# Performance work log

Hardware: AMD Instinct MI355X
Metric: run time of the kernel (lower is better)

## Reference

```python
import jax, jax.numpy as jnp
import numpy as np

B, T, D = 2048, 60, 6
H, F, O = 64, 10, 1


def setup_inputs() -> dict:
    key = jax.random.key(0)
    ks = jax.random.split(key, 16)
    w = lambda k, shape, s=0.1: jax.random.normal(k, shape, jnp.float32) * s
    return {
        "x": jax.random.normal(ks[0], (B, T, D), jnp.float32),
        "W_i": w(ks[1], (D, H)), "U_i": w(ks[2], (H, H)), "b_i": jnp.zeros((H,), jnp.float32),
        "W_ste": w(ks[3], (D, H)), "U_ste": w(ks[4], (H, H)), "b_ste": jnp.ones((H,), jnp.float32),
        "W_fre": w(ks[5], (D, F)), "U_fre": w(ks[6], (H, F)), "b_fre": jnp.ones((F,), jnp.float32),
        "W_c": w(ks[7], (D, H)), "U_c": w(ks[8], (H, H)), "b_c": jnp.zeros((H,), jnp.float32),
        "W_o": w(ks[9], (D, H)), "U_o": w(ks[10], (H, H)), "b_o": jnp.zeros((H,), jnp.float32),
        "U_a": w(ks[11], (F, 1)), "b_a": jnp.zeros((H,), jnp.float32),
        "W_p": w(ks[12], (H, O)), "b_p": jnp.zeros((O,), jnp.float32),
    }


def _hsig(v):
    # torch.nn.Hardsigmoid: relu6(x + 3) / 6
    return jnp.clip(v / 6.0 + 0.5, 0.0, 1.0)


def reference(x, W_i, U_i, b_i, W_ste, U_ste, b_ste, W_fre, U_fre, b_fre,
              W_c, U_c, b_c, W_o, U_o, b_o, U_a, b_a, W_p, b_p):
    b, t_len, _ = x.shape
    h_dim = W_i.shape[1]
    f_dim = W_fre.shape[1]
    freq = jnp.arange(f_dim, dtype=x.dtype) / f_dim  # (F,)
    ua = U_a[:, 0]  # (F,)

    def step(carry, x_t):
        h, S_re, S_im, t = carry
        i = _hsig(x_t @ W_i + b_i + h @ U_i)              # (B,H)
        ste = _hsig(x_t @ W_ste + b_ste + h @ U_ste)      # (B,H)
        fre = _hsig(x_t @ W_fre + b_fre + h @ U_fre)      # (B,F)
        f = ste[:, :, None] * fre[:, None, :]             # (B,H,F)
        c = i * jnp.tanh(x_t @ W_c + b_c + h @ U_c)       # (B,H)
        t = t + 1.0
        omega = (2.0 * jnp.pi) * t * freq                  # (F,)
        S_re = f * S_re + c[:, :, None] * jnp.cos(omega)   # (B,H,F)
        S_im = f * S_im + c[:, :, None] * jnp.sin(omega)   # (B,H,F)
        A = S_re * S_re + S_im * S_im                      # (B,H,F)
        a = jnp.tanh(jnp.einsum('bhf,f->bh', A, ua) + b_a)
        o = _hsig(x_t @ W_o + b_o + h @ U_o)
        h = o * a
        return (h, S_re, S_im, t), None

    init = (jnp.zeros((b, h_dim), x.dtype),
            jnp.zeros((b, h_dim, f_dim), x.dtype),
            jnp.zeros((b, h_dim, f_dim), x.dtype),
            jnp.asarray(0.0, x.dtype))
    (h, _, _, _), _ = jax.lax.scan(step, init, jnp.swapaxes(x, 0, 1))
    # original returns p from the last timestep only
    return h @ W_p + b_p
```

## Files before the change

kernel.cpp:

```cpp
#include <hip/hip_runtime.h>


#define BB 2048
#define TT 60
#define DD 6
#define HH 64
#define FF 10
#define NB 8

#define XS 968
#define HS 72

typedef short bf16x8 __attribute__((ext_vector_type(8)));
typedef float f32x4  __attribute__((ext_vector_type(4)));

__device__ __forceinline__ unsigned short f2bf(float f) {
    union { float f; unsigned u; } v; v.f = f;
    unsigned r = v.u + 0x7fffu + ((v.u >> 16) & 1u);
    return (unsigned short)(r >> 16);
}
__device__ __forceinline__ float bf2f(unsigned short b) {
    union { unsigned u; float f; } v; v.u = ((unsigned)b) << 16; return v.f;
}
__device__ __forceinline__ float hsig_f(float v) {
    return __builtin_amdgcn_fmed3f(fmaf(v, 0.16666666666666666f, 0.5f), 0.0f, 1.0f);
}
__device__ __forceinline__ float tanh_f(float x) {
    float xc = fminf(fmaxf(x, -12.0f), 12.0f);
    float e  = __builtin_amdgcn_exp2f(xc * 2.8853900817779268f);
    return (e - 1.0f) * __builtin_amdgcn_rcpf(e + 1.0f);
}
__device__ __forceinline__ float uni(float v) {
    return __int_as_float(__builtin_amdgcn_readfirstlane(__float_as_int(v)));
}
__device__ __forceinline__ void pinv(bf16x8& v) { asm volatile("" : "+v"(v)); }

__global__ __launch_bounds__(512, 2)
void sfm_kernel(
    const float* __restrict__ x,
    const float* __restrict__ W_i,  const float* __restrict__ U_i,  const float* __restrict__ b_i,
    const float* __restrict__ W_ste,const float* __restrict__ U_ste,const float* __restrict__ b_ste,
    const float* __restrict__ W_fre,const float* __restrict__ U_fre,const float* __restrict__ b_fre,
    const float* __restrict__ W_c,  const float* __restrict__ U_c,  const float* __restrict__ b_c,
    const float* __restrict__ W_o,  const float* __restrict__ U_o,  const float* __restrict__ b_o,
    const float* __restrict__ U_a,  const float* __restrict__ b_a,
    const float* __restrict__ W_p,  const float* __restrict__ b_p,
    float* __restrict__ out)
{
    const int tid  = threadIdx.x;
    const int lane = tid & 63;
    const int wave = tid >> 6;
    const int q    = lane >> 4;
    const int n16  = lane & 15;
    const int b0   = blockIdx.x * NB;

    __shared__ __align__(16) unsigned short xsp[NB * XS];
    __shared__ __align__(16) unsigned short hhi[NB * HS];
    __shared__ __align__(16) unsigned short hlo[NB * HS];
    __shared__ __align__(16) float zbuf[4 * 64 * NB];
    __shared__ __align__(16) float frebuf[16 * NB];
    __shared__ float red[8][NB];

    if (tid < NB * TT) {
        const float* xg = x + (size_t)b0 * (TT * DD) + tid * DD;
        const int b = tid / TT, s = tid - b * TT;
        unsigned short* dst = &xsp[b * XS + s * 16];
        #pragma unroll
        for (int d = 0; d < DD; ++d) {
            const float v = xg[d];
            const unsigned short hb = f2bf(v);
            dst[d]     = hb;
            dst[8 + d] = f2bf(v - bf2f(hb));
        }
        dst[6] = 0x3F80; dst[7] = 0;
        dst[14] = 0; dst[15] = 0;
    }
    for (int i = tid; i < NB * HS; i += 512) { hhi[i] = 0; hlo[i] = 0; }

    const int g = wave >> 1;
    const int colbase = (wave & 1) * 32;
    const float* Ug = (g == 0) ? U_i : (g == 1) ? U_ste : (g == 2) ? U_c : U_o;
    const float* Wg = (g == 0) ? W_i : (g == 1) ? W_ste : (g == 2) ? W_c : W_o;
    const float* bg = (g == 0) ? b_i : (g == 1) ? b_ste : (g == 2) ? b_c : b_o;

    bf16x8 Bh[3][3], Bl[3][3];
    #pragma unroll
    for (int t = 0; t < 3; ++t) {
        #pragma unroll
        for (int c = 0; c < 3; ++c) {
            #pragma unroll
            for (int j = 0; j < 8; ++j) {
                const int kv = c * 32 + q * 8 + j;
                float v = 0.0f;
                if (t < 2) {
                    const int n = colbase + t * 16 + n16;
                    if      (kv < 64)  v = Ug[kv * HH + n];
                    else if (kv < 70)  v = Wg[(kv - 64) * HH + n];
                    else if (kv == 70) v = bg[n];
                } else if (wave == 7 && n16 < FF) {
                    if      (kv < 64)  v = U_fre[kv * FF + n16];
                    else if (kv < 70)  v = W_fre[(kv - 64) * FF + n16];
                    else if (kv == 70) v = b_fre[n16];
                }
                const unsigned short hb = f2bf(v);
                Bh[t][c][j] = (short)hb;
                Bl[t][c][j] = (short)f2bf(v - bf2f(hb));
            }
            pinv(Bh[t][c]); pinv(Bl[t][c]);
        }
    }

    const int pb = tid & (NB - 1);
    const int pc = tid >> 3;
    const float bav = b_a[pc];
    const float wpv = W_p[pc];
    const float bpv = uni(b_p[0]);
    float uav[FF];
    #pragma unroll
    for (int f = 0; f < FF; ++f) uav[f] = uni(U_a[f]);

    const float CBt[FF] = { 1.0f,  0.8090169943749475f,  0.30901699437494745f,
                           -0.30901699437494745f, -0.8090169943749475f, -1.0f,
                           -0.8090169943749475f, -0.30901699437494745f,
                            0.30901699437494745f,  0.8090169943749475f };
    const float SBt[FF] = { 0.0f,  0.5877852522924731f,  0.9510565162951535f,
                            0.9510565162951535f,  0.5877852522924731f,  0.0f,
                           -0.5877852522924731f, -0.9510565162951535f,
                           -0.9510565162951535f, -0.5877852522924731f };

    float Sre[FF], Sim[FF], cs[FF], sn[FF];
    #pragma unroll
    for (int f = 0; f < FF; ++f) {
        Sre[f] = 0.0f; Sim[f] = 0.0f; cs[f] = CBt[f]; sn[f] = SBt[f];
    }
    float hv = 0.0f;

    const int ab = n16 & (NB - 1);
    const unsigned short* hhp = &hhi[ab * HS];
    const unsigned short* hlp = &hlo[ab * HS];
    const unsigned short* xrow = &xsp[ab * XS];

    __syncthreads();

    int sm = 0;
    for (int s = 0; s < TT; ++s) {
        bf16x8 Ah[3], Al[3];
        #pragma unroll
        for (int c = 0; c < 2; ++c) {
            Ah[c] = *(const bf16x8*)&hhp[c * 32 + q * 8];
            Al[c] = *(const bf16x8*)&hlp[c * 32 + q * 8];
        }
        {
            const bf16x8 xvh = *(const bf16x8*)&xrow[s * 16];
            const bf16x8 xvl = *(const bf16x8*)&xrow[s * 16 + 8];
            const bf16x8 zf = {0, 0, 0, 0, 0, 0, 0, 0};
            Ah[2] = (q == 0) ? xvh : zf;
            Al[2] = (q == 0) ? xvl : zf;
        }

        f32x4 acc0 = {0.f,0.f,0.f,0.f}, acc1 = acc0, acc2 = acc0;
        #pragma unroll
        for (int c = 0; c < 3; ++c) {
            #pragma unroll
            for (int tm = 0; tm < 3; ++tm) {
                const bf16x8 a = (tm == 0) ? Al[c] : Ah[c];
                acc0 = __builtin_amdgcn_mfma_f32_16x16x32_bf16(a, (tm==1) ? Bl[0][c] : Bh[0][c], acc0, 0, 0, 0);
                acc1 = __builtin_amdgcn_mfma_f32_16x16x32_bf16(a, (tm==1) ? Bl[1][c] : Bh[1][c], acc1, 0, 0, 0);
                if (wave == 7)
                    acc2 = __builtin_amdgcn_mfma_f32_16x16x32_bf16(a, (tm==1) ? Bl[2][c] : Bh[2][c], acc2, 0, 0, 0);
            }
        }

        if (q < 2) {
            const int base = (g * 64 + colbase + n16) * NB + q * 4;
            *(f32x4*)&zbuf[base]          = acc0;
            *(f32x4*)&zbuf[base + 16*NB]  = acc1;
            if (wave == 7)
                *(f32x4*)&frebuf[n16 * NB + q * 4] = acc2;
        }
        __syncthreads();

        const float zi = zbuf[(0 * 64 + pc) * NB + pb];
        const float zs = zbuf[(1 * 64 + pc) * NB + pb];
        const float zc = zbuf[(2 * 64 + pc) * NB + pb];
        const float zo = zbuf[(3 * 64 + pc) * NB + pb];
        float fr[FF];
        #pragma unroll
        for (int f = 0; f < FF; ++f) fr[f] = hsig_f(frebuf[f * NB + pb]);

        const float iv  = hsig_f(zi);
        const float stv = hsig_f(zs);
        const float ov  = hsig_f(zo);
        const float cv  = iv * tanh_f(zc);

        if (sm == 0) {
            #pragma unroll
            for (int f = 0; f < FF; ++f) { cs[f] = CBt[f]; sn[f] = SBt[f]; }
        }

        float aacc = bav;
        #pragma unroll
        for (int f = 0; f < FF; ++f) {
            const float fc = stv * fr[f];
            Sre[f] = fmaf(fc, Sre[f], cv * cs[f]);
            Sim[f] = fmaf(fc, Sim[f], cv * sn[f]);
            const float A = fmaf(Sim[f], Sim[f], Sre[f] * Sre[f]);
            aacc = fmaf(A, uav[f], aacc);
            const float cc = cs[f];
            cs[f] = fmaf(cc, CBt[f], -(sn[f] * SBt[f]));
            sn[f] = fmaf(cc, SBt[f],   sn[f] * CBt[f]);
        }
        hv = ov * tanh_f(aacc);

        {
            const unsigned short hb = f2bf(hv);
            hhi[pb * HS + pc] = hb;
            hlo[pb * HS + pc] = f2bf(hv - bf2f(hb));
        }
        if (++sm == 10) sm = 0;
        __syncthreads();
    }

    float val = hv * wpv;
    val += __shfl_xor(val, 8, 64);
    val += __shfl_xor(val, 16, 64);
    val += __shfl_xor(val, 32, 64);
    if (lane < NB) red[wave][lane] = val;
    __syncthreads();
    if (tid < NB) {
        float acc = bpv;
        #pragma unroll
        for (int w = 0; w < 8; ++w) acc += red[w][tid];
        out[b0 + tid] = acc;
    }
}

extern "C" void kernel_launch(void* const* d_in, const int* in_sizes, int n_in,
                              void* d_out, int out_size, void* d_ws, size_t ws_size,
                              hipStream_t stream) {
    (void)in_sizes; (void)n_in; (void)d_ws; (void)ws_size; (void)out_size;
    const float* x     = (const float*)d_in[0];
    const float* W_i   = (const float*)d_in[1];
    const float* U_i   = (const float*)d_in[2];
    const float* b_i   = (const float*)d_in[3];
    const float* W_ste = (const float*)d_in[4];
    const float* U_ste = (const float*)d_in[5];
    const float* b_ste = (const float*)d_in[6];
    const float* W_fre = (const float*)d_in[7];
    const float* U_fre = (const float*)d_in[8];
    const float* b_fre = (const float*)d_in[9];
    const float* W_c   = (const float*)d_in[10];
    const float* U_c   = (const float*)d_in[11];
    const float* b_c   = (const float*)d_in[12];
    const float* W_o   = (const float*)d_in[13];
    const float* U_o   = (const float*)d_in[14];
    const float* b_o   = (const float*)d_in[15];
    const float* U_a   = (const float*)d_in[16];
    const float* b_a   = (const float*)d_in[17];
    const float* W_p   = (const float*)d_in[18];
    const float* b_p   = (const float*)d_in[19];

    sfm_kernel<<<BB / NB, 512, 0, stream>>>(
        x, W_i, U_i, b_i, W_ste, U_ste, b_ste, W_fre, U_fre, b_fre,
        W_c, U_c, b_c, W_o, U_o, b_o, U_a, b_a, W_p, b_p, (float*)d_out);
}
```

Baseline: 163.7 us.

## Transpose MFMA roles: weights as A operand, hi/lo hidden state stacked in N

Swaps the MFMA operands so the weight tiles are held in registers as the A operand. The hidden state's bf16 hi and lo halves are stacked as 16 N-columns, and the two partial sums are added when the gate inputs are read back. This drops from 9 MFMAs per tile to 6 per step and removes the per-lane A-fragment gathers. It also replaces the per-step cos/sin rotation recurrence with a shared-memory lookup table, splits the attention accumulation into two chains, and lowers the launch-bounds occupancy hint from 2 to 1. In exchange it adds an extra shared-memory read per gate, a shuffle for the frequency gate, and table loads in the inner loop.

```diff
diff --git a/kernel.cpp b/kernel.cpp
--- a/kernel.cpp
+++ b/kernel.cpp
@@ -9,7 +9,8 @@
 #define NB 8
 
 #define XS 968
-#define HS 72
+#define HSK 72
+#define ZC 68
 
 typedef short bf16x8 __attribute__((ext_vector_type(8)));
 typedef float f32x4  __attribute__((ext_vector_type(4)));
@@ -35,7 +36,7 @@
 }
 __device__ __forceinline__ void pinv(bf16x8& v) { asm volatile("" : "+v"(v)); }
 
-__global__ __launch_bounds__(512, 2)
+__global__ __launch_bounds__(512, 1)
 void sfm_kernel(
     const float* __restrict__ x,
     const float* __restrict__ W_i,  const float* __restrict__ U_i,  const float* __restrict__ b_i,
@@ -55,11 +56,12 @@
     const int b0   = blockIdx.x * NB;
 
     __shared__ __align__(16) unsigned short xsp[NB * XS];
-    __shared__ __align__(16) unsigned short hhi[NB * HS];
-    __shared__ __align__(16) unsigned short hlo[NB * HS];
-    __shared__ __align__(16) float zbuf[4 * 64 * NB];
-    __shared__ __align__(16) float frebuf[16 * NB];
-    __shared__ float red[8][NB];
+    __shared__ __align__(16) unsigned short hsp2[16 * HSK];
+    __shared__ __align__(16) float zt[4 * 16 * ZC];
+    __shared__ __align__(16) float fb[NB * 12];
+    __shared__ __align__(16) float ctab[10 * 10 * 2];
+    __shared__ float cstabB[10 * 2];
+    __shared__ float red[8][8];
 
     if (tid < NB * TT) {
         const float* xg = x + (size_t)b0 * (TT * DD) + tid * DD;
@@ -75,42 +77,65 @@
         dst[6] = 0x3F80; dst[7] = 0;
         dst[14] = 0; dst[15] = 0;
     }
-    for (int i = tid; i < NB * HS; i += 512) { hhi[i] = 0; hlo[i] = 0; }
-
-    const int g = wave >> 1;
-    const int colbase = (wave & 1) * 32;
-    const float* Ug = (g == 0) ? U_i : (g == 1) ? U_ste : (g == 2) ? U_c : U_o;
-    const float* Wg = (g == 0) ? W_i : (g == 1) ? W_ste : (g == 2) ? W_c : W_o;
-    const float* bg = (g == 0) ? b_i : (g == 1) ? b_ste : (g == 2) ? b_c : b_o;
-
-    bf16x8 Bh[3][3], Bl[3][3];
+    if (tid < 10) {
+        const float CTc[10] = { 1.0f,  0.8090169943749475f,  0.30901699437494745f,
+                               -0.30901699437494745f, -0.8090169943749475f, -1.0f,
+                               -0.8090169943749475f, -0.30901699437494745f,
+                                0.30901699437494745f,  0.8090169943749475f };
+        const float STc[10] = { 0.0f,  0.5877852522924731f,  0.9510565162951535f,
+                                0.9510565162951535f,  0.5877852522924731f,  0.0f,
+                               -0.5877852522924731f, -0.9510565162951535f,
+                               -0.9510565162951535f, -0.5877852522924731f };
+        float cc = 0.0f, ss = 0.0f;
+        #pragma unroll
+        for (int j = 0; j < 10; ++j) if (tid == j) { cc = CTc[j]; ss = STc[j]; }
+        cstabB[tid * 2] = cc; cstabB[tid * 2 + 1] = ss;
+    }
+    for (int i = tid; i < 16 * HSK; i += 512) hsp2[i] = 0;
+    __syncthreads();
+    if (tid < 100) {
+        const int mm = tid / 10, ff = tid - mm * 10;
+        const int idx = (ff * mm) % 10;
+        ctab[tid * 2]     = cstabB[idx * 2];
+        ctab[tid * 2 + 1] = cstabB[idx * 2 + 1];
+    }
+
+    const int NTILE = (wave == 7) ? 3 : 2;
+    bf16x8 Ah[3][3], Al[3][3];
     #pragma unroll
     for (int t = 0; t < 3; ++t) {
+        if (t >= NTILE) continue;
+        const bool isfre = (wave == 7 && t == 2);
+        const int gt = 2 * wave + t;
+        const int g  = gt >> 2, mt = gt & 3;
+        const int col = mt * 16 + n16;
+        const float* Ug = (g == 0) ? U_i : (g == 1) ? U_ste : (g == 2) ? U_c : U_o;
+        const float* Wg = (g == 0) ? W_i : (g == 1) ? W_ste : (g == 2) ? W_c : W_o;
+        const float* bg = (g == 0) ? b_i : (g == 1) ? b_ste : (g == 2) ? b_c : b_o;
         #pragma unroll
         for (int c = 0; c < 3; ++c) {
             #pragma unroll
             for (int j = 0; j < 8; ++j) {
                 const int kv = c * 32 + q * 8 + j;
                 float v = 0.0f;
-                if (t < 2) {
-                    const int n = colbase + t * 16 + n16;
-                    if      (kv < 64)  v = Ug[kv * HH + n];
-                    else if (kv < 70)  v = Wg[(kv - 64) * HH + n];
-                    else if (kv == 70) v = bg[n];
-                } else if (wave == 7 && n16 < FF) {
+                if (!isfre) {
+                    if      (kv < 64)  v = Ug[kv * HH + col];
+                    else if (kv < 70)  v = Wg[(kv - 64) * HH + col];
+                    else if (kv == 70) v = bg[col];
+                } else if (n16 < FF) {
                     if      (kv < 64)  v = U_fre[kv * FF + n16];
                     else if (kv < 70)  v = W_fre[(kv - 64) * FF + n16];
                     else if (kv == 70) v = b_fre[n16];
                 }
                 const unsigned short hb = f2bf(v);
-                Bh[t][c][j] = (short)hb;
-                Bl[t][c][j] = (short)f2bf(v - bf2f(hb));
+                Ah[t][c][j] = (short)hb;
+                Al[t][c][j] = (short)f2bf(v - bf2f(hb));
             }
-            pinv(Bh[t][c]); pinv(Bl[t][c]);
-        }
-    }
-
-    const int pb = tid & (NB - 1);
+            pinv(Ah[t][c]); pinv(Al[t][c]);
+        }
+    }
+
+    const int pb = tid & 7;
     const int pc = tid >> 3;
     const float bav = b_a[pc];
     const float wpv = W_p[pc];
@@ -119,105 +144,93 @@
     #pragma unroll
     for (int f = 0; f < FF; ++f) uav[f] = uni(U_a[f]);
 
-    const float CBt[FF] = { 1.0f,  0.8090169943749475f,  0.30901699437494745f,
-                           -0.30901699437494745f, -0.8090169943749475f, -1.0f,
-                           -0.8090169943749475f, -0.30901699437494745f,
-                            0.30901699437494745f,  0.8090169943749475f };
-    const float SBt[FF] = { 0.0f,  0.5877852522924731f,  0.9510565162951535f,
-                            0.9510565162951535f,  0.5877852522924731f,  0.0f,
-                           -0.5877852522924731f, -0.9510565162951535f,
-                           -0.9510565162951535f, -0.5877852522924731f };
-
-    float Sre[FF], Sim[FF], cs[FF], sn[FF];
+    float Sre[FF], Sim[FF];
     #pragma unroll
-    for (int f = 0; f < FF; ++f) {
-        Sre[f] = 0.0f; Sim[f] = 0.0f; cs[f] = CBt[f]; sn[f] = SBt[f];
-    }
+    for (int f = 0; f < FF; ++f) { Sre[f] = 0.0f; Sim[f] = 0.0f; }
     float hv = 0.0f;
 
-    const int ab = n16 & (NB - 1);
-    const unsigned short* hhp = &hhi[ab * HS];
-    const unsigned short* hlp = &hlo[ab * HS];
-    const unsigned short* xrow = &xsp[ab * XS];
+    const unsigned short* hrp = &hsp2[n16 * HSK];
+    const unsigned short* xrp = &xsp[(n16 & 7) * XS + (n16 >> 3) * 8];
 
     __syncthreads();
 
-    int sm = 0;
+    int m = 1;
     for (int s = 0; s < TT; ++s) {
-        bf16x8 Ah[3], Al[3];
-        #pragma unroll
-        for (int c = 0; c < 2; ++c) {
-            Ah[c] = *(const bf16x8*)&hhp[c * 32 + q * 8];
-            Al[c] = *(const bf16x8*)&hlp[c * 32 + q * 8];
-        }
-        {
-            const bf16x8 xvh = *(const bf16x8*)&xrow[s * 16];
-            const bf16x8 xvl = *(const bf16x8*)&xrow[s * 16 + 8];
-            const bf16x8 zf = {0, 0, 0, 0, 0, 0, 0, 0};
-            Ah[2] = (q == 0) ? xvh : zf;
-            Al[2] = (q == 0) ? xvl : zf;
-        }
-
-        f32x4 acc0 = {0.f,0.f,0.f,0.f}, acc1 = acc0, acc2 = acc0;
-        #pragma unroll
-        for (int c = 0; c < 3; ++c) {
+        const bf16x8 B0 = *(const bf16x8*)&hrp[q * 8];
+        const bf16x8 B1 = *(const bf16x8*)&hrp[32 + q * 8];
+        const bf16x8 xv = *(const bf16x8*)&xrp[s * 16];
+        const bf16x8 zf = {0, 0, 0, 0, 0, 0, 0, 0};
+        const bf16x8 B2 = (q == 0) ? xv : zf;
+
+        f32x4 acc[3];
+        #pragma unroll
+        for (int t = 0; t < 3; ++t) {
+            if (t >= NTILE) continue;
+            f32x4 a = {0.0f, 0.0f, 0.0f, 0.0f};
+            a = __builtin_amdgcn_mfma_f32_16x16x32_bf16(Ah[t][0], B0, a, 0, 0, 0);
+            a = __builtin_amdgcn_mfma_f32_16x16x32_bf16(Al[t][0], B0, a, 0, 0, 0);
+            a = __builtin_amdgcn_mfma_f32_16x16x32_bf16(Ah[t][1], B1, a, 0, 0, 0);
+            a = __builtin_amdgcn_mfma_f32_16x16x32_bf16(Al[t][1], B1, a, 0, 0, 0);
+            a = __builtin_amdgcn_mfma_f32_16x16x32_bf16(Ah[t][2], B2, a, 0, 0, 0);
+            a = __builtin_amdgcn_mfma_f32_16x16x32_bf16(Al[t][2], B2, a, 0, 0, 0);
+            acc[t] = a;
+        }
+
+        #pragma unroll
+        for (int t = 0; t < 2; ++t) {
+            const int gt = 2 * wave + t;
+            const int g  = gt >> 2, mt = gt & 3;
+            *(f32x4*)&zt[(g * 16 + n16) * ZC + mt * 16 + q * 4] = acc[t];
+        }
+        if (wave == 7) {
+            f32x4 af;
             #pragma unroll
-            for (int tm = 0; tm < 3; ++tm) {
-                const bf16x8 a = (tm == 0) ? Al[c] : Ah[c];
-                acc0 = __builtin_amdgcn_mfma_f32_16x16x32_bf16(a, (tm==1) ? Bl[0][c] : Bh[0][c], acc0, 0, 0, 0);
-                acc1 = __builtin_amdgcn_mfma_f32_16x16x32_bf16(a, (tm==1) ? Bl[1][c] : Bh[1][c], acc1, 0, 0, 0);
-                if (wave == 7)
-                    acc2 = __builtin_amdgcn_mfma_f32_16x16x32_bf16(a, (tm==1) ? Bl[2][c] : Bh[2][c], acc2, 0, 0, 0);
+            for (int r = 0; r < 4; ++r)
+                af[r] = acc[2][r] + __shfl_xor(acc[2][r], 8, 64);
+            if (n16 < 8) {
+                #pragma unroll
+                for (int r = 0; r < 4; ++r) {
+                    const int f = q * 4 + r;
+                    if (f < FF) fb[n16 * 12 + f] = af[r];
+                }
             }
         }
-
-        if (q < 2) {
-            const int base = (g * 64 + colbase + n16) * NB + q * 4;
-            *(f32x4*)&zbuf[base]          = acc0;
-            *(f32x4*)&zbuf[base + 16*NB]  = acc1;
-            if (wave == 7)
-                *(f32x4*)&frebuf[n16 * NB + q * 4] = acc2;
-        }
         __syncthreads();
 
-        const float zi = zbuf[(0 * 64 + pc) * NB + pb];
-        const float zs = zbuf[(1 * 64 + pc) * NB + pb];
-        const float zc = zbuf[(2 * 64 + pc) * NB + pb];
-        const float zo = zbuf[(3 * 64 + pc) * NB + pb];
+        const float zi = zt[(0 * 16 + pb) * ZC + pc] + zt[(0 * 16 + pb + 8) * ZC + pc];
+        const float zs = zt[(1 * 16 + pb) * ZC + pc] + zt[(1 * 16 + pb + 8) * ZC + pc];
+        const float zc = zt[(2 * 16 + pb) * ZC + pc] + zt[(2 * 16 + pb + 8) * ZC + pc];
+        const float zo = zt[(3 * 16 + pb) * ZC + pc] + zt[(3 * 16 + pb + 8) * ZC + pc];
+
         float fr[FF];
         #pragma unroll
-        for (int f = 0; f < FF; ++f) fr[f] = hsig_f(frebuf[f * NB + pb]);
+        for (int f = 0; f < FF; ++f) fr[f] = hsig_f(fb[pb * 12 + f]);
 
         const float iv  = hsig_f(zi);
         const float stv = hsig_f(zs);
         const float ov  = hsig_f(zo);
         const float cv  = iv * tanh_f(zc);
 
-        if (sm == 0) {
-            #pragma unroll
-            for (int f = 0; f < FF; ++f) { cs[f] = CBt[f]; sn[f] = SBt[f]; }
-        }
-
-        float aacc = bav;
+        const float* tp = &ctab[m * 20];
+        float aacc0 = bav, aacc1 = 0.0f;
         #pragma unroll
         for (int f = 0; f < FF; ++f) {
+            const float2 tv = *(const float2*)&tp[f * 2];
             const float fc = stv * fr[f];
-            Sre[f] = fmaf(fc, Sre[f], cv * cs[f]);
-            Sim[f] = fmaf(fc, Sim[f], cv * sn[f]);
+            Sre[f] = fmaf(fc, Sre[f], cv * tv.x);
+            Sim[f] = fmaf(fc, Sim[f], cv * tv.y);
             const float A = fmaf(Sim[f], Sim[f], Sre[f] * Sre[f]);
-            aacc = fmaf(A, uav[f], aacc);
-            const float cc = cs[f];
-            cs[f] = fmaf(cc, CBt[f], -(sn[f] * SBt[f]));
-            sn[f] = fmaf(cc, SBt[f],   sn[f] * CBt[f]);
-        }
-        hv = ov * tanh_f(aacc);
+            if (f & 1) aacc1 = fmaf(A, uav[f], aacc1);
+            else       aacc0 = fmaf(A, uav[f], aacc0);
+        }
+        hv = ov * tanh_f(aacc0 + aacc1);
 
         {
             const unsigned short hb = f2bf(hv);
-            hhi[pb * HS + pc] = hb;
-            hlo[pb * HS + pc] = f2bf(hv - bf2f(hb));
-        }
-        if (++sm == 10) sm = 0;
+            hsp2[pb * HSK + pc]       = hb;
+            hsp2[(8 + pb) * HSK + pc] = f2bf(hv - bf2f(hb));
+        }
+        if (++m == 10) m = 0;
         __syncthreads();
     }
 
@@ -225,7 +238,7 @@
     val += __shfl_xor(val, 8, 64);
     val += __shfl_xor(val, 16, 64);
     val += __shfl_xor(val, 32, 64);
-    if (lane < NB) red[wave][lane] = val;
+    if (lane < 8) red[wave][lane] = val;
     __syncthreads();
     if (tid < NB) {
         float acc = bpv;
```

Result: faster. 157.1 us (-4.0%).
